# Kernel tuning notes

Measured on AMD Instinct MI355X. Metric: run time of the kernel, lower is better.

Reference implementation:

```python
import jax, jax.numpy as jnp
import numpy as np

EMB_DIM = 1024
HEAD = 16
HEAD_DIM = EMB_DIM // HEAD


def setup_inputs() -> dict:
    key = jax.random.key(0)
    ks = jax.random.split(key, 6)
    s = 1.0 / np.sqrt(EMB_DIM)
    return {
        "z": jax.random.normal(ks[0], (4, 2048, EMB_DIM), dtype=jnp.float32),
        "w_q": jax.random.normal(ks[1], (EMB_DIM, EMB_DIM), dtype=jnp.float32) * s,
        "w_k": jax.random.normal(ks[2], (EMB_DIM, EMB_DIM), dtype=jnp.float32) * s,
        "w_v": jax.random.normal(ks[3], (EMB_DIM, EMB_DIM), dtype=jnp.float32) * s,
        "w_o": jax.random.normal(ks[4], (EMB_DIM, EMB_DIM), dtype=jnp.float32) * s,
        "b_o": jax.random.normal(ks[5], (EMB_DIM,), dtype=jnp.float32) * 0.01,
    }


def reference(z, w_q, w_k, w_v, w_o, b_o):
    B, N, D = z.shape
    # QKV projections (nn.Linear: x @ W.T; here weights stored as (D_in, D_out))
    q = (z @ w_q).reshape(B, N, HEAD, HEAD_DIM).transpose(0, 2, 1, 3)  # bhnd
    k = (z @ w_k).reshape(B, N, HEAD, HEAD_DIM).transpose(0, 2, 1, 3)
    v = (z @ w_v).reshape(B, N, HEAD, HEAD_DIM).transpose(0, 2, 1, 3)
    scale = 1.0 / np.sqrt(HEAD_DIM).astype(np.float32)
    dots = jnp.einsum("bhnd,bhmd->bhnm", q, k) * scale
    attn = jax.nn.softmax(dots, axis=-1)
    out = jnp.einsum("bhnm,bhmd->bhnd", attn, v)
    out = out.transpose(0, 2, 1, 3).reshape(B, N, D)
    return out @ w_o + b_o
```

## Files before the change

### kernel.cpp

```cpp
#include <hip/hip_runtime.h>
#include <hip/hip_bf16.h>
#include <stdint.h>

typedef unsigned short u16;
typedef __attribute__((ext_vector_type(8))) short bf16x8;
typedef __attribute__((ext_vector_type(4))) float f32x4;
typedef __attribute__((ext_vector_type(16))) float f32x16;

static __device__ inline u16 f2bf(float f) {
  union { float f; uint32_t u; } v; v.f = f;
  uint32_t u = v.u;
  u += 0x7fffu + ((u >> 16) & 1);
  return (u16)(u >> 16);
}

static __device__ inline float fast_exp2(float x) {
#if __has_builtin(__builtin_amdgcn_exp2f)
  return __builtin_amdgcn_exp2f(x);
#else
  return __expf(x * 0.6931471805599453f);
#endif
}

static __device__ inline uint32_t pack_bf16(float lo, float hi) {
#if __has_builtin(__builtin_amdgcn_cvt_pk_bf16_f32)
  typedef __attribute__((ext_vector_type(2))) __bf16 bf16x2_t;
  bf16x2_t r = __builtin_amdgcn_cvt_pk_bf16_f32(lo, hi);
  union { bf16x2_t v; uint32_t u; } c; c.v = r;
  return c.u;
#else
  union { float f; uint32_t u; } a, b;
  a.f = lo; b.f = hi;
  uint32_t ua = a.u + 0x8000u;
  uint32_t ub = b.u + 0x8000u;
  return __builtin_amdgcn_perm(ub, ua, 0x07060302u);
#endif
}

static __device__ __forceinline__ void plswap(uint32_t a, uint32_t b,
                                              uint32_t& x, uint32_t& y) {
#if __has_builtin(__builtin_amdgcn_permlane32_swap)
  auto r = __builtin_amdgcn_permlane32_swap(a, b, false, false);
  x = (uint32_t)r[0]; y = (uint32_t)r[1];
#else
  int h = (threadIdx.x & 63) >> 5;
  uint32_t pa = (uint32_t)__shfl_xor((int)a, 32, 64);
  uint32_t pb = (uint32_t)__shfl_xor((int)b, 32, 64);
  x = h ? pb : a;
  y = h ? b : pa;
#endif
}

static __device__ __forceinline__ void load_lds_128(const u16* g, u16* l) {
  __builtin_amdgcn_global_load_lds((const __attribute__((address_space(1))) void*)g,
                                   (__attribute__((address_space(3))) void*)l,
                                   16, 0, 0);
}

__global__ __launch_bounds__(256) void prep_kernel(const float* __restrict__ zsrc,
                                                   u16* __restrict__ zdst,
                                                   const float* __restrict__ wq,
                                                   const float* __restrict__ wk,
                                                   const float* __restrict__ wv,
                                                   const float* __restrict__ wo,
                                                   u16* __restrict__ bqkv,
                                                   u16* __restrict__ wot) {
  const int bid = blockIdx.x;
  const int tid = threadIdx.x;
  if (bid < 8192) {
    int i = bid * 256 + tid;
    float4 v = reinterpret_cast<const float4*>(zsrc)[i];
    uint2 o;
    o.x = pack_bf16(v.x, v.y);
    o.y = pack_bf16(v.z, v.w);
    reinterpret_cast<uint2*>(zdst)[i] = o;
    return;
  }
  const int w = bid - 8192;
  const int z = w >> 10;
  const int rem = w & 1023;
  const float* src = (z == 0) ? wq : (z == 1) ? wk : (z == 2) ? wv : wo;
  u16* dst = (z < 3) ? (bqkv + (size_t)z * 1024 * 1024) : wot;
  __shared__ float tile[32][33];
  const int c0 = (rem & 31) * 32, r0 = (rem >> 5) * 32;
  const int tx = tid & 31, ty = tid >> 5;
#pragma unroll
  for (int i = 0; i < 32; i += 8)
    tile[ty + i][tx] = src[(size_t)(r0 + ty + i) * 1024 + c0 + tx];
  __syncthreads();
#pragma unroll
  for (int i = 0; i < 32; i += 8)
    dst[(size_t)(c0 + ty + i) * 1024 + r0 + tx] = f2bf(tile[tx][ty + i]);
}

__global__ __launch_bounds__(256) void gemm_bt64_kernel(
    const u16* __restrict__ A, const u16* __restrict__ Bt,
    float* __restrict__ outC, const float* __restrict__ bias) {
  const int Kd = 1024;
  unsigned lin = blockIdx.y * gridDim.x + blockIdx.x;
  unsigned nwg = gridDim.x * gridDim.y;
  lin = (lin & 7u) * (nwg >> 3) + (lin >> 3);
  const int n0 = (lin % gridDim.x) * 64;
  const int m0 = (lin / gridDim.x) * 128;
  __shared__ __align__(16) u16 Asm[128 * 32];
  __shared__ __align__(16) u16 Bsm[64 * 32];
  const int tid = threadIdx.x;
  const int wave = tid >> 6, lane = tid & 63;
  const int quad = lane >> 4, l15 = lane & 15;
  const int wm = (wave >> 1) * 64, wn = (wave & 1) * 32;

  const int c0 = wave * 128 + lane;
  const int c1 = c0 + 64;
  const int r0 = c0 >> 2, p0 = (c0 & 3) * 8;
  const int r1 = c1 >> 2, p1 = (c1 & 3) * 8;
  const int cB = tid;
  const int rB = cB >> 2, pB = (cB & 3) * 8;

  const u16* Ab = A + (size_t)m0 * Kd;
  const u16* Bb = Bt + (size_t)n0 * Kd;

  f32x4 acc[4][2] = {};

  for (int k0 = 0; k0 < Kd; k0 += 32) {
    __syncthreads();
    load_lds_128(Ab + (size_t)r0 * Kd + k0 + p0, Asm + c0 * 8);
    load_lds_128(Ab + (size_t)r1 * Kd + k0 + p1, Asm + c1 * 8);
    load_lds_128(Bb + (size_t)rB * Kd + k0 + pB, Bsm + cB * 8);
    __syncthreads();
    bf16x8 af[4], bf[2];
#pragma unroll
    for (int i = 0; i < 4; i++)
      af[i] = *reinterpret_cast<const bf16x8*>(Asm + (wm + i * 16 + l15) * 32 + quad * 8);
#pragma unroll
    for (int i = 0; i < 2; i++)
      bf[i] = *reinterpret_cast<const bf16x8*>(Bsm + (wn + i * 16 + l15) * 32 + quad * 8);
#pragma unroll
    for (int mi = 0; mi < 4; mi++)
#pragma unroll
      for (int ni = 0; ni < 2; ni++)
        acc[mi][ni] = __builtin_amdgcn_mfma_f32_16x16x32_bf16(af[mi], bf[ni], acc[mi][ni], 0, 0, 0);
  }

#pragma unroll
  for (int mi = 0; mi < 4; mi++)
#pragma unroll
    for (int ni = 0; ni < 2; ni++) {
      int n = n0 + wn + ni * 16 + l15;
      float bv = bias[n];
#pragma unroll
      for (int r = 0; r < 4; r++) {
        int m = m0 + wm + mi * 16 + quad * 4 + r;
        outC[(size_t)m * 1024 + n] = acc[mi][ni][r] + bv;
      }
    }
}

template <int VT>
__global__ __launch_bounds__(512, 2) void gemm256_kernel(
    const u16* __restrict__ A, const u16* __restrict__ Bt,
    u16* __restrict__ outQ, u16* __restrict__ outK, u16* __restrict__ outVt) {
  const int tid = threadIdx.x;
  const int lane = tid & 63;
  const int wave = tid >> 6;
  const int quad = lane >> 4, l15 = lane & 15;
  const int e15 = l15 & 7;
  const int wm = wave >> 2;
  const int wn = wave & 3;

  unsigned lin = blockIdx.y * gridDim.x + blockIdx.x;
  unsigned nwg = gridDim.x * gridDim.y;
  lin = (lin & 7u) * (nwg >> 3) + (lin >> 3);
  const int bx = lin % gridDim.x, by = lin / gridDim.x;
  const int n0 = (VT ? 2048 : 0) + bx * 256;
  const int m0 = by * 256;

  __shared__ __align__(16) u16 AsmL[2][16384];
  __shared__ __align__(16) u16 BsmL[2][16384];
  u16* const As_[2] = {&AsmL[0][0], &AsmL[1][0]};
  u16* const Bs_[2] = {&BsmL[0][0], &BsmL[1][0]};

  const u16* Abase = A + (size_t)m0 * 1024;
  const u16* Bbase = Bt + (size_t)n0 * 1024;

  const int awoff = wm * 8192;
  const int bwoff = (wn >> 1) * 8192 + (wn & 1) * 4096;

  f32x4 acc[8][4] = {};
  bf16x8 af[4][2], bfr[4][2];

#define STG_HALF(ldsp, gp)                                                      \
  {                                                                             \
    const int cs0 = tid, cs1 = tid + 512;                                       \
    const int r0_ = cs0 >> 3, g0_ = (((cs0 & 7) ^ (r0_ & 7)) << 3);             \
    const int r1_ = cs1 >> 3, g1_ = (((cs1 & 7) ^ (r1_ & 7)) << 3);             \
    load_lds_128((gp) + (size_t)r0_ * 1024 + g0_, (ldsp) + cs0 * 8);            \
    load_lds_128((gp) + (size_t)r1_ * 1024 + g1_, (ldsp) + cs1 * 8);            \
  }

#define PHB() do { asm volatile("" ::: "memory"); __builtin_amdgcn_s_barrier(); \
                   asm volatile("" ::: "memory"); } while (0)
#define LGKM0() do { asm volatile("s_waitcnt lgkmcnt(0)" ::: "memory");         \
                     __builtin_amdgcn_sched_barrier(0); } while (0)
#define VMC8()  asm volatile("s_waitcnt vmcnt(8)" ::: "memory")

#define RD_A(mb, B)                                                             \
  _Pragma("unroll") for (int x = 0; x < 4; x++)                                 \
  _Pragma("unroll") for (int kk = 0; kk < 2; kk++)                              \
    af[x][kk] = *reinterpret_cast<const bf16x8*>(                               \
        As_[B] + awoff + (((mb) + x) * 16 + l15) * 64 + (((quad + kk * 4) ^ e15) << 3));

#define RD_B(nb, B)                                                             \
  _Pragma("unroll") for (int x = 0; x < 2; x++)                                 \
  _Pragma("unroll") for (int kk = 0; kk < 2; kk++)                              \
    bfr[(nb) + x][kk] = *reinterpret_cast<const bf16x8*>(                       \
        Bs_[B] + bwoff + (((nb) + x) * 16 + l15) * 64 + (((quad + kk * 4) ^ e15) << 3));

#define MM(mb, nb)                                                              \
  _Pragma("unroll") for (int kk = 0; kk < 2; kk++)                              \
  _Pragma("unroll") for (int x = 0; x < 4; x++)                                 \
  _Pragma("unroll") for (int y = 0; y < 2; y++) {                               \
    if (VT)                                                                     \
      acc[(mb) + x][(nb) + y] = __builtin_amdgcn_mfma_f32_16x16x32_bf16(        \
          af[x][kk], bfr[(nb) + y][kk], acc[(mb) + x][(nb) + y], 0, 0, 0);      \
    else                                                                        \
      acc[(mb) + x][(nb) + y] = __builtin_amdgcn_mfma_f32_16x16x32_bf16(        \
          bfr[(nb) + y][kk], af[x][kk], acc[(mb) + x][(nb) + y], 0, 0, 0);      \
  }

#define TILE4(B, KS)                                                            \
  RD_A(0, B); RD_B(0, B);                                                       \
  PHB(); LGKM0(); __builtin_amdgcn_s_setprio(1); MM(0, 0);                      \
  __builtin_amdgcn_s_setprio(0); PHB();                                         \
  RD_B(2, B);                                                                   \
  PHB(); LGKM0(); __builtin_amdgcn_s_setprio(1); MM(0, 2);                      \
  __builtin_amdgcn_s_setprio(0); PHB();                                         \
  RD_A(4, B);                                                                   \
  STG_HALF(Bs_[B], Bbase + (KS)); STG_HALF(Bs_[B] + 8192, Bbase + 128 * 1024 + (KS)); \
  PHB(); LGKM0(); __builtin_amdgcn_s_setprio(1); MM(4, 0);                      \
  __builtin_amdgcn_s_setprio(0); PHB();                                         \
  STG_HALF(As_[B], Abase + (KS)); STG_HALF(As_[B] + 8192, Abase + 128 * 1024 + (KS)); \
  PHB(); __builtin_amdgcn_s_setprio(1); MM(4, 2);                               \
  __builtin_amdgcn_s_setprio(0); VMC8(); PHB();

  STG_HALF(As_[0], Abase);      STG_HALF(As_[0] + 8192, Abase + 128 * 1024);
  STG_HALF(Bs_[0], Bbase);      STG_HALF(Bs_[0] + 8192, Bbase + 128 * 1024);
  STG_HALF(As_[1], Abase + 64); STG_HALF(As_[1] + 8192, Abase + 128 * 1024 + 64);
  STG_HALF(Bs_[1], Bbase + 64); STG_HALF(Bs_[1] + 8192, Bbase + 128 * 1024 + 64);
  VMC8(); PHB();

#pragma unroll 1
  for (int it = 0; it < 8; ++it) {
    int t2 = it * 2 + 2; if (t2 > 15) t2 = 15;
    int t3 = it * 2 + 3; if (t3 > 15) t3 = 15;
    const int k2 = t2 * 64, k3 = t3 * 64;
    TILE4(0, k2);
    TILE4(1, k3);
  }

  if (VT) {
#pragma unroll
    for (int mi = 0; mi < 8; mi++)
#pragma unroll
      for (int ni = 0; ni < 4; ni++) {
        int n = n0 + wn * 64 + ni * 16 + l15;
        int hn = n & 1023;
        int hh = hn >> 6, dim = hn & 63;
        int m = m0 + wm * 128 + mi * 16 + quad * 4;
        int b = m >> 11, tok = m & 2047;
        uint2 pk;
        pk.x = pack_bf16(acc[mi][ni][0], acc[mi][ni][1]);
        pk.y = pack_bf16(acc[mi][ni][2], acc[mi][ni][3]);
        *reinterpret_cast<uint2*>(outVt + ((size_t)(b * 16 + hh) * 64 + dim) * 2048 + tok) = pk;
      }
  } else {
    const int which = (n0 + wn * 64) >> 10;
    u16* dst0 = which ? outK : outQ;
    const float qscale = which ? 1.0f : 0.1803368801111204f;
    const int hh = ((n0 + wn * 64) & 1023) >> 6;
#pragma unroll
    for (int mi = 0; mi < 8; mi++) {
      int mrow = m0 + wm * 128 + mi * 16 + l15;
      int b = mrow >> 11, tok = mrow & 2047;
      u16* drow = dst0 + ((size_t)(b * 16 + hh) * 2048 + tok) * 64;
#pragma unroll
      for (int ni = 0; ni < 4; ni++) {
        int dim0 = ni * 16 + quad * 4;
        uint2 o;
        o.x = pack_bf16(acc[mi][ni][0] * qscale, acc[mi][ni][1] * qscale);
        o.y = pack_bf16(acc[mi][ni][2] * qscale, acc[mi][ni][3] * qscale);
        *reinterpret_cast<uint2*>(drow + dim0) = o;
      }
    }
  }
#undef STG_HALF
#undef PHB
#undef LGKM0
#undef VMC8
#undef RD_A
#undef RD_B
#undef MM
#undef TILE4
}

__global__ __launch_bounds__(256, 2) void attn_kernel(const u16* __restrict__ Q,
                                                      const u16* __restrict__ K,
                                                      const u16* __restrict__ Vt,
                                                      u16* __restrict__ Oout) {
  const int bh = blockIdx.x;
  const int q0 = blockIdx.y * 256;
  const int tid = threadIdx.x;
  const int wave = tid >> 6, lane = tid & 63;
  const int l31 = lane & 31, h = lane >> 5;
  const int e = l31 & 7;

  __shared__ __align__(16) u16 Kb2[2][4096];
  __shared__ __align__(16) u16 Vb2[2][4096];

  const u16* Qg = Q + ((size_t)bh * 2048 + q0 + wave * 64) * 64;
  const u16* Kg = K + (size_t)bh * 2048 * 64;
  const u16* Vg = Vt + (size_t)bh * 64 * 2048;

  bf16x8 qf[2][4];
#pragma unroll
  for (int j = 0; j < 2; j++)
#pragma unroll
    for (int dc = 0; dc < 4; dc++)
      qf[j][dc] = *reinterpret_cast<const bf16x8*>(
          Qg + (size_t)(j * 32 + l31) * 64 + dc * 16 + h * 8);

  const int s0 = tid, s1 = tid + 256;
  const int sr0 = s0 >> 3, sg0 = ((s0 & 7) ^ (sr0 & 7)) * 8;
  const int sr1 = s1 >> 3, sg1 = ((s1 & 7) ^ (sr1 & 7)) * 8;

  load_lds_128(Kg + (size_t)sr0 * 64 + sg0, &Kb2[0][s0 * 8]);
  load_lds_128(Kg + (size_t)sr1 * 64 + sg1, &Kb2[0][s1 * 8]);
  load_lds_128(Vg + (size_t)sr0 * 2048 + sg0, &Vb2[0][s0 * 8]);
  load_lds_128(Vg + (size_t)sr1 * 2048 + sg1, &Vb2[0][s1 * 8]);
  __syncthreads();

  float ls[2][2] = {};
  f32x16 oacc[2][2] = {};
  int cur = 0;

  for (int kt = 0; kt < 2048; kt += 64) {
    const u16* uK = &Kb2[cur][0];
    const u16* uV = &Vb2[cur][0];

    bf16x8 kfr[2][4], vfr[2][2][2];
#pragma unroll
    for (int kb = 0; kb < 2; kb++)
#pragma unroll
      for (int dc = 0; dc < 4; dc++)
        kfr[kb][dc] = *reinterpret_cast<const bf16x8*>(
            uK + (kb * 32 + l31) * 64 + (((2 * dc + h) ^ e) * 8));
#pragma unroll
    for (int dt = 0; dt < 2; dt++)
#pragma unroll
      for (int kb = 0; kb < 2; kb++)
#pragma unroll
        for (int kc = 0; kc < 2; kc++)
          vfr[dt][kb][kc] = *reinterpret_cast<const bf16x8*>(
              uV + (dt * 32 + l31) * 64 + (((4 * kb + 2 * kc + h) ^ e) * 8));

    if (kt + 64 < 2048) {
      const int nb = cur ^ 1;
      load_lds_128(Kg + (size_t)(kt + 64 + sr0) * 64 + sg0, &Kb2[nb][s0 * 8]);
      load_lds_128(Kg + (size_t)(kt + 64 + sr1) * 64 + sg1, &Kb2[nb][s1 * 8]);
      load_lds_128(Vg + (size_t)sr0 * 2048 + kt + 64 + sg0, &Vb2[nb][s0 * 8]);
      load_lds_128(Vg + (size_t)sr1 * 2048 + kt + 64 + sg1, &Vb2[nb][s1 * 8]);
    }

    f32x16 s4[4];
    __builtin_amdgcn_s_setprio(1);
#pragma unroll
    for (int g = 0; g < 4; g++) {
      const int kb = g >> 1, j = g & 1;
      f32x16 s = {};
#pragma unroll
      for (int dc = 0; dc < 4; dc++)
        s = __builtin_amdgcn_mfma_f32_32x32x16_bf16(kfr[kb][dc], qf[j][dc], s, 0, 0, 0);
      s4[g] = s;
    }
    __builtin_amdgcn_s_setprio(0);

#pragma unroll
    for (int g = 0; g < 4; g++) {
      const int kb = g >> 1, j = g & 1;
      float p[16];
#pragma unroll
      for (int i = 0; i < 16; i++) p[i] = fast_exp2(s4[g][i]);
#pragma unroll
      for (int i = 0; i < 16; i += 2) { ls[j][0] += p[i]; ls[j][1] += p[i + 1]; }
      uint32_t pk[4][2];
#pragma unroll
      for (int rq = 0; rq < 4; rq++) {
        pk[rq][0] = pack_bf16(p[rq * 4 + 0], p[rq * 4 + 1]);
        pk[rq][1] = pack_bf16(p[rq * 4 + 2], p[rq * 4 + 3]);
      }
      uint4 b0, b1;
      plswap(pk[0][0], pk[1][0], b0.x, b0.z);
      plswap(pk[0][1], pk[1][1], b0.y, b0.w);
      plswap(pk[2][0], pk[3][0], b1.x, b1.z);
      plswap(pk[2][1], pk[3][1], b1.y, b1.w);
      union { uint4 u; bf16x8 v; } bf0, bf1;
      bf0.u = b0; bf1.u = b1;
      __builtin_amdgcn_s_setprio(1);
#pragma unroll
      for (int dt = 0; dt < 2; dt++) {
        oacc[j][dt] = __builtin_amdgcn_mfma_f32_32x32x16_bf16(vfr[dt][kb][0], bf0.v, oacc[j][dt], 0, 0, 0);
        oacc[j][dt] = __builtin_amdgcn_mfma_f32_32x32x16_bf16(vfr[dt][kb][1], bf1.v, oacc[j][dt], 0, 0, 0);
      }
      __builtin_amdgcn_s_setprio(0);
    }

    __syncthreads();
    cur ^= 1;
  }

  const int b = bh >> 4, hd = bh & 15;
  u16* dst = Oout + (size_t)b * 2048 * 1024 + (size_t)hd * 64;
#pragma unroll
  for (int j = 0; j < 2; j++) {
    float lsum = ls[j][0] + ls[j][1];
    lsum += __shfl_xor(lsum, 32, 64);
    float inv = __builtin_amdgcn_rcpf(lsum);
    const size_t qrow = (size_t)(q0 + wave * 64 + j * 32 + l31) * 1024;
#pragma unroll
    for (int dt = 0; dt < 2; dt++)
#pragma unroll
      for (int rq = 0; rq < 4; rq++) {
        uint2 o;
        o.x = pack_bf16(oacc[j][dt][rq * 4 + 0] * inv, oacc[j][dt][rq * 4 + 1] * inv);
        o.y = pack_bf16(oacc[j][dt][rq * 4 + 2] * inv, oacc[j][dt][rq * 4 + 3] * inv);
        *reinterpret_cast<uint2*>(dst + qrow + dt * 32 + rq * 8 + h * 4) = o;
      }
  }
}

extern "C" void kernel_launch(void* const* d_in, const int* in_sizes, int n_in,
                              void* d_out, int out_size, void* d_ws, size_t ws_size,
                              hipStream_t stream) {
  (void)in_sizes; (void)n_in; (void)out_size; (void)ws_size;
  const float* z  = (const float*)d_in[0];
  const float* wq = (const float*)d_in[1];
  const float* wk = (const float*)d_in[2];
  const float* wv = (const float*)d_in[3];
  const float* wo = (const float*)d_in[4];
  const float* bo = (const float*)d_in[5];
  float* out = (float*)d_out;

  char* ws = (char*)d_ws;
  u16* zb   = (u16*)(ws);
  u16* bqkv = (u16*)(ws + (16ull << 20));
  u16* wot  = (u16*)(ws + (22ull << 20));
  u16* Qb   = (u16*)(ws + (24ull << 20));
  u16* Kb   = (u16*)(ws + (40ull << 20));
  u16* Vtb  = (u16*)(ws + (56ull << 20));
  u16* Ob   = zb;

  prep_kernel<<<12288, 256, 0, stream>>>(z, zb, wq, wk, wv, wo, bqkv, wot);
  gemm256_kernel<0><<<dim3(8, 32), 512, 0, stream>>>(zb, bqkv, Qb, Kb, Vtb);
  gemm256_kernel<1><<<dim3(4, 32), 512, 0, stream>>>(zb, bqkv, Qb, Kb, Vtb);
  attn_kernel<<<dim3(64, 8), 256, 0, stream>>>(Qb, Kb, Vtb, Ob);
  gemm_bt64_kernel<<<dim3(16, 64), 256, 0, stream>>>(Ob, wot, out, bo);
}
```

Baseline: 287.4 us.

## Merge QK and V projection launches; widen output GEMM K-step with swizzled LDS

The separate Q/K and V projection launches become one 12x32 grid kernel that branches per block on column range, using a templated k-loop with swapped MFMA operand order for the Q/K path. This removes one launch and the tail of the smaller V grid. The output projection GEMM now stages 64-wide K tiles with XOR-swizzled LDS addressing, which halves its barrier count and reduces bank conflicts. It also drops the block-index remap, which may change L2 locality.

Result: no change. 283.4 us (-1.4%).

```diff
diff --git a/kernel.cpp b/kernel.cpp
--- a/kernel.cpp
+++ b/kernel.cpp
@@ -97,48 +97,65 @@
     const u16* __restrict__ A, const u16* __restrict__ Bt,
     float* __restrict__ outC, const float* __restrict__ bias) {
   const int Kd = 1024;
-  unsigned lin = blockIdx.y * gridDim.x + blockIdx.x;
-  unsigned nwg = gridDim.x * gridDim.y;
-  lin = (lin & 7u) * (nwg >> 3) + (lin >> 3);
-  const int n0 = (lin % gridDim.x) * 64;
-  const int m0 = (lin / gridDim.x) * 128;
-  __shared__ __align__(16) u16 Asm[128 * 32];
-  __shared__ __align__(16) u16 Bsm[64 * 32];
+  const int n0 = blockIdx.x * 64;
+  const int m0 = blockIdx.y * 128;
+  __shared__ __align__(16) u16 Asm[128 * 64];
+  __shared__ __align__(16) u16 Bsm[64 * 64];
   const int tid = threadIdx.x;
   const int wave = tid >> 6, lane = tid & 63;
   const int quad = lane >> 4, l15 = lane & 15;
+  const int e15 = l15 & 7;
   const int wm = (wave >> 1) * 64, wn = (wave & 1) * 32;
 
-  const int c0 = wave * 128 + lane;
-  const int c1 = c0 + 64;
-  const int r0 = c0 >> 2, p0 = (c0 & 3) * 8;
-  const int r1 = c1 >> 2, p1 = (c1 & 3) * 8;
-  const int cB = tid;
-  const int rB = cB >> 2, pB = (cB & 3) * 8;
+  int rA[4], gA[4];
+#pragma unroll
+  for (int i = 0; i < 4; i++) {
+    int c = tid + i * 256;
+    rA[i] = c >> 3;
+    gA[i] = (((c & 7) ^ (rA[i] & 7)) << 3);
+  }
+  int rB[2], gB[2];
+#pragma unroll
+  for (int i = 0; i < 2; i++) {
+    int c = tid + i * 256;
+    rB[i] = c >> 3;
+    gB[i] = (((c & 7) ^ (rB[i] & 7)) << 3);
+  }
 
   const u16* Ab = A + (size_t)m0 * Kd;
   const u16* Bb = Bt + (size_t)n0 * Kd;
 
   f32x4 acc[4][2] = {};
 
-  for (int k0 = 0; k0 < Kd; k0 += 32) {
+  for (int k0 = 0; k0 < Kd; k0 += 64) {
     __syncthreads();
-    load_lds_128(Ab + (size_t)r0 * Kd + k0 + p0, Asm + c0 * 8);
-    load_lds_128(Ab + (size_t)r1 * Kd + k0 + p1, Asm + c1 * 8);
-    load_lds_128(Bb + (size_t)rB * Kd + k0 + pB, Bsm + cB * 8);
+#pragma unroll
+    for (int i = 0; i < 4; i++)
+      load_lds_128(Ab + (size_t)rA[i] * Kd + k0 + gA[i], Asm + (tid + i * 256) * 8);
+#pragma unroll
+    for (int i = 0; i < 2; i++)
+      load_lds_128(Bb + (size_t)rB[i] * Kd + k0 + gB[i], Bsm + (tid + i * 256) * 8);
     __syncthreads();
-    bf16x8 af[4], bf[2];
-#pragma unroll
-    for (int i = 0; i < 4; i++)
-      af[i] = *reinterpret_cast<const bf16x8*>(Asm + (wm + i * 16 + l15) * 32 + quad * 8);
-#pragma unroll
-    for (int i = 0; i < 2; i++)
-      bf[i] = *reinterpret_cast<const bf16x8*>(Bsm + (wn + i * 16 + l15) * 32 + quad * 8);
-#pragma unroll
-    for (int mi = 0; mi < 4; mi++)
-#pragma unroll
-      for (int ni = 0; ni < 2; ni++)
-        acc[mi][ni] = __builtin_amdgcn_mfma_f32_16x16x32_bf16(af[mi], bf[ni], acc[mi][ni], 0, 0, 0);
+    bf16x8 af[4][2], bf[2][2];
+#pragma unroll
+    for (int x = 0; x < 4; x++)
+#pragma unroll
+      for (int kk = 0; kk < 2; kk++)
+        af[x][kk] = *reinterpret_cast<const bf16x8*>(
+            Asm + (wm + x * 16 + l15) * 64 + (((quad + kk * 4) ^ e15) << 3));
+#pragma unroll
+    for (int y = 0; y < 2; y++)
+#pragma unroll
+      for (int kk = 0; kk < 2; kk++)
+        bf[y][kk] = *reinterpret_cast<const bf16x8*>(
+            Bsm + (wn + y * 16 + l15) * 64 + (((quad + kk * 4) ^ e15) << 3));
+#pragma unroll
+    for (int kk = 0; kk < 2; kk++)
+#pragma unroll
+      for (int mi = 0; mi < 4; mi++)
+#pragma unroll
+        for (int ni = 0; ni < 2; ni++)
+          acc[mi][ni] = __builtin_amdgcn_mfma_f32_16x16x32_bf16(af[mi][kk], bf[ni][kk], acc[mi][ni], 0, 0, 0);
   }
 
 #pragma unroll
@@ -154,39 +171,6 @@
       }
     }
 }
-
-template <int VT>
-__global__ __launch_bounds__(512, 2) void gemm256_kernel(
-    const u16* __restrict__ A, const u16* __restrict__ Bt,
-    u16* __restrict__ outQ, u16* __restrict__ outK, u16* __restrict__ outVt) {
-  const int tid = threadIdx.x;
-  const int lane = tid & 63;
-  const int wave = tid >> 6;
-  const int quad = lane >> 4, l15 = lane & 15;
-  const int e15 = l15 & 7;
-  const int wm = wave >> 2;
-  const int wn = wave & 3;
-
-  unsigned lin = blockIdx.y * gridDim.x + blockIdx.x;
-  unsigned nwg = gridDim.x * gridDim.y;
-  lin = (lin & 7u) * (nwg >> 3) + (lin >> 3);
-  const int bx = lin % gridDim.x, by = lin / gridDim.x;
-  const int n0 = (VT ? 2048 : 0) + bx * 256;
-  const int m0 = by * 256;
-
-  __shared__ __align__(16) u16 AsmL[2][16384];
-  __shared__ __align__(16) u16 BsmL[2][16384];
-  u16* const As_[2] = {&AsmL[0][0], &AsmL[1][0]};
-  u16* const Bs_[2] = {&BsmL[0][0], &BsmL[1][0]};
-
-  const u16* Abase = A + (size_t)m0 * 1024;
-  const u16* Bbase = Bt + (size_t)n0 * 1024;
-
-  const int awoff = wm * 8192;
-  const int bwoff = (wn >> 1) * 8192 + (wn & 1) * 4096;
-
-  f32x4 acc[8][4] = {};
-  bf16x8 af[4][2], bfr[4][2];
 
 #define STG_HALF(ldsp, gp)                                                      \
   {                                                                             \
@@ -196,37 +180,32 @@
     load_lds_128((gp) + (size_t)r0_ * 1024 + g0_, (ldsp) + cs0 * 8);            \
     load_lds_128((gp) + (size_t)r1_ * 1024 + g1_, (ldsp) + cs1 * 8);            \
   }
-
 #define PHB() do { asm volatile("" ::: "memory"); __builtin_amdgcn_s_barrier(); \
                    asm volatile("" ::: "memory"); } while (0)
 #define LGKM0() do { asm volatile("s_waitcnt lgkmcnt(0)" ::: "memory");         \
                      __builtin_amdgcn_sched_barrier(0); } while (0)
 #define VMC8()  asm volatile("s_waitcnt vmcnt(8)" ::: "memory")
-
 #define RD_A(mb, B)                                                             \
   _Pragma("unroll") for (int x = 0; x < 4; x++)                                 \
   _Pragma("unroll") for (int kk = 0; kk < 2; kk++)                              \
     af[x][kk] = *reinterpret_cast<const bf16x8*>(                               \
         As_[B] + awoff + (((mb) + x) * 16 + l15) * 64 + (((quad + kk * 4) ^ e15) << 3));
-
 #define RD_B(nb, B)                                                             \
   _Pragma("unroll") for (int x = 0; x < 2; x++)                                 \
   _Pragma("unroll") for (int kk = 0; kk < 2; kk++)                              \
     bfr[(nb) + x][kk] = *reinterpret_cast<const bf16x8*>(                       \
         Bs_[B] + bwoff + (((nb) + x) * 16 + l15) * 64 + (((quad + kk * 4) ^ e15) << 3));
-
 #define MM(mb, nb)                                                              \
   _Pragma("unroll") for (int kk = 0; kk < 2; kk++)                              \
   _Pragma("unroll") for (int x = 0; x < 4; x++)                                 \
   _Pragma("unroll") for (int y = 0; y < 2; y++) {                               \
-    if (VT)                                                                     \
+    if (SWAPQK)                                                                 \
+      acc[(mb) + x][(nb) + y] = __builtin_amdgcn_mfma_f32_16x16x32_bf16(        \
+          bfr[(nb) + y][kk], af[x][kk], acc[(mb) + x][(nb) + y], 0, 0, 0);      \
+    else                                                                        \
       acc[(mb) + x][(nb) + y] = __builtin_amdgcn_mfma_f32_16x16x32_bf16(        \
           af[x][kk], bfr[(nb) + y][kk], acc[(mb) + x][(nb) + y], 0, 0, 0);      \
-    else                                                                        \
-      acc[(mb) + x][(nb) + y] = __builtin_amdgcn_mfma_f32_16x16x32_bf16(        \
-          bfr[(nb) + y][kk], af[x][kk], acc[(mb) + x][(nb) + y], 0, 0, 0);      \
-  }
-
+  }
 #define TILE4(B, KS)                                                            \
   RD_A(0, B); RD_B(0, B);                                                       \
   PHB(); LGKM0(); __builtin_amdgcn_s_setprio(1); MM(0, 0);                      \
@@ -242,6 +221,14 @@
   PHB(); __builtin_amdgcn_s_setprio(1); MM(4, 2);                               \
   __builtin_amdgcn_s_setprio(0); VMC8(); PHB();
 
+template <bool SWAPQK>
+static __device__ __forceinline__ void gemm256_kloop(
+    const u16* Abase, const u16* Bbase, u16* As0, u16* As1, u16* Bs0, u16* Bs1,
+    int tid, int l15, int quad, int e15, int awoff, int bwoff, f32x4 (&acc)[8][4]) {
+  u16* const As_[2] = {As0, As1};
+  u16* const Bs_[2] = {Bs0, Bs1};
+  bf16x8 af[4][2], bfr[4][2];
+
   STG_HALF(As_[0], Abase);      STG_HALF(As_[0] + 8192, Abase + 128 * 1024);
   STG_HALF(Bs_[0], Bbase);      STG_HALF(Bs_[0] + 8192, Bbase + 128 * 1024);
   STG_HALF(As_[1], Abase + 64); STG_HALF(As_[1] + 8192, Abase + 128 * 1024 + 64);
@@ -256,8 +243,60 @@
     TILE4(0, k2);
     TILE4(1, k3);
   }
-
-  if (VT) {
+}
+
+__global__ __launch_bounds__(512, 2) void gemm256_kernel(
+    const u16* __restrict__ A, const u16* __restrict__ Bt,
+    u16* __restrict__ outQ, u16* __restrict__ outK, u16* __restrict__ outVt) {
+  const int tid = threadIdx.x;
+  const int lane = tid & 63;
+  const int wave = tid >> 6;
+  const int quad = lane >> 4, l15 = lane & 15;
+  const int e15 = l15 & 7;
+  const int wm = wave >> 2;
+  const int wn = wave & 3;
+
+  unsigned lin = blockIdx.y * gridDim.x + blockIdx.x;
+  unsigned nwg = gridDim.x * gridDim.y;
+  lin = (lin & 7u) * (nwg >> 3) + (lin >> 3);
+  const int bx = lin % gridDim.x, by = lin / gridDim.x;
+  const int n0 = bx * 256, m0 = by * 256;
+
+  __shared__ __align__(16) u16 AsmL[2][16384];
+  __shared__ __align__(16) u16 BsmL[2][16384];
+
+  const u16* Abase = A + (size_t)m0 * 1024;
+  const u16* Bbase = Bt + (size_t)n0 * 1024;
+
+  const int awoff = wm * 8192;
+  const int bwoff = (wn >> 1) * 8192 + (wn & 1) * 4096;
+
+  f32x4 acc[8][4] = {};
+
+  if (n0 < 2048) {
+    gemm256_kloop<true>(Abase, Bbase, &AsmL[0][0], &AsmL[1][0], &BsmL[0][0], &BsmL[1][0],
+                        tid, l15, quad, e15, awoff, bwoff, acc);
+    const int which = (n0 + wn * 64) >> 10;
+    u16* dst0 = which ? outK : outQ;
+    const float qscale = which ? 1.0f : 0.1803368801111204f;
+    const int hh = ((n0 + wn * 64) & 1023) >> 6;
+#pragma unroll
+    for (int mi = 0; mi < 8; mi++) {
+      int mrow = m0 + wm * 128 + mi * 16 + l15;
+      int b = mrow >> 11, tok = mrow & 2047;
+      u16* drow = dst0 + ((size_t)(b * 16 + hh) * 2048 + tok) * 64;
+#pragma unroll
+      for (int ni = 0; ni < 4; ni++) {
+        int dim0 = ni * 16 + quad * 4;
+        uint2 o;
+        o.x = pack_bf16(acc[mi][ni][0] * qscale, acc[mi][ni][1] * qscale);
+        o.y = pack_bf16(acc[mi][ni][2] * qscale, acc[mi][ni][3] * qscale);
+        *reinterpret_cast<uint2*>(drow + dim0) = o;
+      }
+    }
+  } else {
+    gemm256_kloop<false>(Abase, Bbase, &AsmL[0][0], &AsmL[1][0], &BsmL[0][0], &BsmL[1][0],
+                         tid, l15, quad, e15, awoff, bwoff, acc);
 #pragma unroll
     for (int mi = 0; mi < 8; mi++)
 #pragma unroll
@@ -272,26 +311,8 @@
         pk.y = pack_bf16(acc[mi][ni][2], acc[mi][ni][3]);
         *reinterpret_cast<uint2*>(outVt + ((size_t)(b * 16 + hh) * 64 + dim) * 2048 + tok) = pk;
       }
-  } else {
-    const int which = (n0 + wn * 64) >> 10;
-    u16* dst0 = which ? outK : outQ;
-    const float qscale = which ? 1.0f : 0.1803368801111204f;
-    const int hh = ((n0 + wn * 64) & 1023) >> 6;
-#pragma unroll
-    for (int mi = 0; mi < 8; mi++) {
-      int mrow = m0 + wm * 128 + mi * 16 + l15;
-      int b = mrow >> 11, tok = mrow & 2047;
-      u16* drow = dst0 + ((size_t)(b * 16 + hh) * 2048 + tok) * 64;
-#pragma unroll
-      for (int ni = 0; ni < 4; ni++) {
-        int dim0 = ni * 16 + quad * 4;
-        uint2 o;
-        o.x = pack_bf16(acc[mi][ni][0] * qscale, acc[mi][ni][1] * qscale);
-        o.y = pack_bf16(acc[mi][ni][2] * qscale, acc[mi][ni][3] * qscale);
-        *reinterpret_cast<uint2*>(drow + dim0) = o;
-      }
-    }
-  }
+  }
+}
 #undef STG_HALF
 #undef PHB
 #undef LGKM0
@@ -300,7 +321,6 @@
 #undef RD_B
 #undef MM
 #undef TILE4
-}
 
 __global__ __launch_bounds__(256, 2) void attn_kernel(const u16* __restrict__ Q,
                                                       const u16* __restrict__ K,
@@ -459,8 +479,7 @@
   u16* Ob   = zb;
 
   prep_kernel<<<12288, 256, 0, stream>>>(z, zb, wq, wk, wv, wo, bqkv, wot);
-  gemm256_kernel<0><<<dim3(8, 32), 512, 0, stream>>>(zb, bqkv, Qb, Kb, Vtb);
-  gemm256_kernel<1><<<dim3(4, 32), 512, 0, stream>>>(zb, bqkv, Qb, Kb, Vtb);
+  gemm256_kernel<<<dim3(12, 32), 512, 0, stream>>>(zb, bqkv, Qb, Kb, Vtb);
   attn_kernel<<<dim3(64, 8), 256, 0, stream>>>(Qb, Kb, Vtb, Ob);
   gemm_bt64_kernel<<<dim3(16, 64), 256, 0, stream>>>(Ob, wot, out, bo);
 }
```
